# Kernel optimization log

Measured on AMD Instinct MI355X. Metric: run time of the kernel, lower is better.

The kernel has to match this reference:

```python
import jax, jax.numpy as jnp
import numpy as np


def setup_inputs() -> dict:
    key = jax.random.key(0)
    k1, k2, k3, k4 = jax.random.split(key, 4)
    B, N, M, C = 2, 16384, 4096, 64
    xyz = jax.random.uniform(k1, (B * N, 3), dtype=jnp.float32) * 10.0
    new_xyz = jax.random.uniform(k2, (B * M, 3), dtype=jnp.float32) * 10.0
    new_xyz_r = jax.random.uniform(k3, (B * M, 1), dtype=jnp.float32) * 0.6 + 0.4
    features = jax.random.normal(k4, (B * N, C), dtype=jnp.float32)
    xyz_batch_cnt = jnp.full((B,), N, dtype=jnp.int32)
    new_xyz_batch_cnt = jnp.full((B,), M, dtype=jnp.int32)
    return {
        "xyz": xyz,
        "xyz_batch_cnt": xyz_batch_cnt,
        "new_xyz": new_xyz,
        "new_xyz_r": new_xyz_r,
        "new_xyz_batch_cnt": new_xyz_batch_cnt,
        "features": features,
        "nsample": 32,
    }


def _ball_query(xyz_b, q_b, r_b, nsample):
    # xyz_b: (B, N, 3), q_b: (B, M, 3), r_b: (B, M)
    # Returns local neighbor indices (B, M, nsample) and empty-ball mask (B, M).
    B, N, _ = xyz_b.shape
    d2 = jnp.sum((q_b[:, :, None, :] - xyz_b[:, None, :, :]) ** 2, axis=-1)  # (B,M,N)
    within = d2 < (r_b[..., None] ** 2)  # (B,M,N)
    # key = point index if within ball else N -> top_k(-key) picks the FIRST
    # nsample in-ball indices in ascending order (matches CUDA ball query).
    pt_idx = jnp.arange(N, dtype=jnp.int32)
    key = jnp.where(within, pt_idx[None, None, :], jnp.int32(N))
    neg_vals, sel = jax.lax.top_k(-key, nsample)  # sel: (B,M,nsample) positions
    count = jnp.sum(within, axis=-1)  # (B,M)
    slot = jnp.arange(nsample, dtype=jnp.int32)
    valid = slot[None, None, :] < count[..., None]
    first = sel[..., 0:1]
    idx = jnp.where(valid, sel, first)  # pad with first found index
    empty = count == 0
    idx = jnp.where(empty[..., None], 0, idx).astype(jnp.int32)
    return idx, empty


def reference(xyz, xyz_batch_cnt, new_xyz, new_xyz_r, new_xyz_batch_cnt, features, nsample):
    B = xyz_batch_cnt.shape[0]
    N = xyz.shape[0] // B  # assumes equal batch counts
    M = new_xyz.shape[0] // B
    C = features.shape[1]
    xyz_b = xyz.reshape(B, N, 3)
    q_b = new_xyz.reshape(B, M, 3)
    r_b = new_xyz_r.reshape(B, M)
    feat_b = features.reshape(B, N, C)

    idx, empty = _ball_query(xyz_b, q_b, r_b, nsample)  # (B,M,ns), (B,M)

    gather = jax.vmap(lambda pts, i: pts[i])  # per-batch gather
    gx = gather(xyz_b, idx)  # (B,M,ns,3)
    grouped_xyz = jnp.transpose(gx, (0, 1, 3, 2)) - q_b[:, :, :, None]  # (B,M,3,ns)
    grouped_xyz = jnp.where(empty[:, :, None, None], 0.0, grouped_xyz)

    gf = gather(feat_b, idx)  # (B,M,ns,C)
    grouped_features = jnp.transpose(gf, (0, 1, 3, 2))  # (B,M,C,ns)
    grouped_features = jnp.where(empty[:, :, None, None], 0.0, grouped_features)

    new_features = jnp.concatenate([grouped_xyz, grouped_features], axis=2)  # use_xyz
    new_features = new_features.reshape(B * M, 3 + C, nsample)
    idx_flat = idx.reshape(B * M, nsample)
    return new_features, idx_flat
```

## Files before the change

kernel.cpp:

```cpp
#include <hip/hip_runtime.h>
#include <hip/hip_bf16.h>

#define NS   32
#define WPB  4
#define GD   10
#define GD3  (GD*GD*GD)
#define CAP  256
#define IMAX 0x7fffffff

__device__ __forceinline__ int clampi(int v, int lo, int hi) {
    return v < lo ? lo : (v > hi ? hi : v);
}

__device__ __forceinline__ int cell_of(float x, float y, float z) {
    const int cx = clampi((int)floorf(x), 0, GD - 1);
    const int cy = clampi((int)floorf(y), 0, GD - 1);
    const int cz = clampi((int)floorf(z), 0, GD - 1);
    return (cz * GD + cy) * GD + cx;
}

__device__ __forceinline__ float dist2_xla(float qx, float qy, float qz,
                                           float x, float y, float z) {
    const float dx = __fsub_rn(qx, x);
    const float dy = __fsub_rn(qy, y);
    const float dz = __fsub_rn(qz, z);
    return __fadd_rn(__fadd_rn(__fmul_rn(dx, dx), __fmul_rn(dy, dy)),
                     __fmul_rn(dz, dz));
}

__device__ __forceinline__ void find_batch(const int* cnts, int B, int p,
                                           int* b_out, int* off_out) {
    int b = 0, off = 0, acc = 0;
    for (int i = 0; i < B; ++i) {
        int c = cnts[i];
        if (p >= acc) { b = i; off = acc; }
        acc += c;
    }
    *b_out = b; *off_out = off;
}


__global__ void count_kernel(const float* __restrict__ xyz,
                             const int* __restrict__ xyz_cnt,
                             int* __restrict__ cnt, int B, int Ntot) {
    const int p = blockIdx.x * blockDim.x + threadIdx.x;
    if (p >= Ntot) return;
    int b, boff; find_batch(xyz_cnt, B, p, &b, &boff);
    const float x = xyz[(size_t)p * 3 + 0];
    const float y = xyz[(size_t)p * 3 + 1];
    const float z = xyz[(size_t)p * 3 + 2];
    atomicAdd(&cnt[b * GD3 + cell_of(x, y, z)], 1);
}

__global__ __launch_bounds__(1024) void prefix_kernel(int* __restrict__ cursor,
                                                      int* __restrict__ cell_start,
                                                      int ncells) {
    __shared__ int s[2048];
    const int t = threadIdx.x;
    for (int i = t; i < 2048; i += 1024) s[i] = (i < ncells) ? cursor[i] : 0;
    __syncthreads();
    for (int off = 1; off < 2048; off <<= 1) {
        const int v0 = s[t];
        const int a0 = (t >= off) ? s[t - off] : 0;
        const int v1 = s[t + 1024];
        const int a1 = s[t + 1024 - off];
        __syncthreads();
        s[t] = v0 + a0;
        s[t + 1024] = v1 + a1;
        __syncthreads();
    }
    for (int i = t; i < ncells; i += 1024) {
        const int excl = (i == 0) ? 0 : s[i - 1];
        cell_start[i] = excl;
        cursor[i]     = excl;
    }
    if (t == 0) cell_start[ncells] = s[ncells - 1];
}

__global__ void scatter_kernel(const float* __restrict__ xyz,
                               const int* __restrict__ xyz_cnt,
                               int* __restrict__ cursor,
                               float4* __restrict__ sorted,
                               int B, int Ntot) {
    const int p = blockIdx.x * blockDim.x + threadIdx.x;
    if (p >= Ntot) return;
    int b, boff; find_batch(xyz_cnt, B, p, &b, &boff);
    const float x = xyz[(size_t)p * 3 + 0];
    const float y = xyz[(size_t)p * 3 + 1];
    const float z = xyz[(size_t)p * 3 + 2];
    const int cell = b * GD3 + cell_of(x, y, z);
    const int slot = atomicAdd(&cursor[cell], 1);
    sorted[slot] = make_float4(x, y, z, __int_as_float(p - boff));
}


__global__ __launch_bounds__(256) void qgp_kernel(
    const float* __restrict__ xyz,
    const int*   __restrict__ xyz_cnt,
    const float* __restrict__ nxyz,
    const float* __restrict__ nr,
    const int*   __restrict__ nxyz_cnt,
    const float* __restrict__ feat,
    const int*   __restrict__ cell_start,
    const float4* __restrict__ sorted,
    float* __restrict__ out_feat,
    float* __restrict__ out_idx,
    int B, int Mtot, int C)
{
    __shared__ int c_list[WPB][CAP];
    __shared__ int idx_buf[WPB][NS];

    const int wv   = threadIdx.x >> 6;
    const int lane = threadIdx.x & 63;
    const int q    = blockIdx.x * WPB + wv;
    if (q >= Mtot) return;

    int b, qoff; find_batch(nxyz_cnt, B, q, &b, &qoff);
    int xoff; { int acc = 0; xoff = 0;
        for (int i = 0; i < B; ++i) { int c = xyz_cnt[i]; if (i == b) xoff = acc; acc += c; } }
    const float* xb = xyz + (size_t)xoff * 3;

    const float qx = nxyz[(size_t)q * 3 + 0];
    const float qy = nxyz[(size_t)q * 3 + 1];
    const float qz = nxyz[(size_t)q * 3 + 2];
    const float r  = nr[q];
    const float r2 = __fmul_rn(r, r);

    const float re = r + 1e-4f;
    const int cx0 = clampi((int)floorf(qx - re), 0, GD - 1);
    const int cx1 = clampi((int)floorf(qx + re), 0, GD - 1);
    const int cy0 = clampi((int)floorf(qy - re), 0, GD - 1);
    const int cy1 = clampi((int)floorf(qy + re), 0, GD - 1);
    const int cz0 = clampi((int)floorf(qz - re), 0, GD - 1);
    const int cz1 = clampi((int)floorf(qz + re), 0, GD - 1);
    const int cbase = b * GD3;

    const unsigned long long lane_mask = (1ull << lane) - 1ull;

    int n = 0;
    for (int cz = cz0; cz <= cz1; ++cz) {
        for (int cy = cy0; cy <= cy1; ++cy) {
            const int rb = cbase + (cz * GD + cy) * GD;
            const int s0 = cell_start[rb + cx0];
            const int s1 = cell_start[rb + cx1 + 1];
            for (int k0 = s0; k0 < s1; k0 += 64) {
                const int k = k0 + lane;
                bool ok = false; int ib = 0;
                if (k < s1) {
                    const float4 P = sorted[k];
                    ok = dist2_xla(qx, qy, qz, P.x, P.y, P.z) < r2;
                    ib = __float_as_int(P.w);
                }
                const unsigned long long m = __ballot(ok);
                if (ok) {
                    const int pos = n + __popcll(m & lane_mask);
                    if (pos < CAP) c_list[wv][pos] = ib;
                }
                n += __popcll(m);
            }
        }
    }
    if (n > CAP) n = CAP;
    __builtin_amdgcn_wave_barrier();

    int c0 = (lane       < n) ? c_list[wv][lane      ] : IMAX;
    int c1 = (lane +  64 < n) ? c_list[wv][lane +  64] : IMAX;
    int c2 = (lane + 128 < n) ? c_list[wv][lane + 128] : IMAX;
    int c3 = (lane + 192 < n) ? c_list[wv][lane + 192] : IMAX;
    const int filled = n < NS ? n : NS;
    for (int i = 0; i < filled; ++i) {
        const int mv = min(min(c0, c1), min(c2, c3));
        int w = mv;
#pragma unroll
        for (int d = 1; d < 64; d <<= 1) w = min(w, __shfl_xor(w, d));
        if (lane == i) idx_buf[wv][i] = w;
        const unsigned long long mm = __ballot(mv == w);
        const int first = __ffsll((unsigned long long)mm) - 1;
        if (lane == first) {
            if      (c0 == w) c0 = IMAX;
            else if (c1 == w) c1 = IMAX;
            else if (c2 == w) c2 = IMAX;
            else              c3 = IMAX;
        }
    }
    __builtin_amdgcn_wave_barrier();

    const bool empty = (n == 0);
    const int cnt32  = filled;
    const int s = lane & 31;
    const int h = lane >> 5;

    int sidx = 0;
    if (!empty) sidx = idx_buf[wv][(s < cnt32) ? s : 0];

    const size_t ob = (size_t)q * (size_t)(3 + C) * NS;

    if (h == 0) {
        out_idx[(size_t)q * NS + s] = (float)sidx;
        float px = 0.f, py = 0.f, pz = 0.f;
        if (!empty) {
            px = __fsub_rn(xb[(size_t)sidx * 3 + 0], qx);
            py = __fsub_rn(xb[(size_t)sidx * 3 + 1], qy);
            pz = __fsub_rn(xb[(size_t)sidx * 3 + 2], qz);
        }
        out_feat[ob + 0 * NS + s] = px;
        out_feat[ob + 1 * NS + s] = py;
        out_feat[ob + 2 * NS + s] = pz;
    }

    const float* frow = feat + (size_t)(xoff + sidx) * C;
    if (C == 64) {
        const float4* frow4 = reinterpret_cast<const float4*>(frow);
#pragma unroll
        for (int j = 0; j < 8; ++j) {
            float4 f;
            if (empty) { f.x = f.y = f.z = f.w = 0.f; }
            else       { f = frow4[h * 8 + j]; }
            const int cb = 3 + h * 32 + j * 4;
            out_feat[ob + (size_t)(cb + 0) * NS + s] = f.x;
            out_feat[ob + (size_t)(cb + 1) * NS + s] = f.y;
            out_feat[ob + (size_t)(cb + 2) * NS + s] = f.z;
            out_feat[ob + (size_t)(cb + 3) * NS + s] = f.w;
        }
    } else {
        for (int c = h; c < C; c += 2) {
            out_feat[ob + (size_t)(3 + c) * NS + s] = empty ? 0.f : frow[c];
        }
    }
}


__global__ __launch_bounds__(256) void qgp_scan_kernel(
    const float* __restrict__ xyz, const int* __restrict__ xyz_cnt,
    const float* __restrict__ nxyz, const float* __restrict__ nr,
    const int* __restrict__ nxyz_cnt, const float* __restrict__ feat,
    float* __restrict__ out_feat, float* __restrict__ out_idx,
    int B, int Mtot, int C)
{
    __shared__ int idx_buf[WPB][NS];
    const int wv = threadIdx.x >> 6, lane = threadIdx.x & 63;
    const int q = blockIdx.x * WPB + wv;
    if (q >= Mtot) return;
    int b, qoff; find_batch(nxyz_cnt, B, q, &b, &qoff);
    int xoff = 0, npts = 0; { int acc = 0;
        for (int i = 0; i < B; ++i) { int c = xyz_cnt[i]; if (i == b) { xoff = acc; npts = c; } acc += c; } }
    const float* xb = xyz + (size_t)xoff * 3;
    const float qx = nxyz[(size_t)q*3], qy = nxyz[(size_t)q*3+1], qz = nxyz[(size_t)q*3+2];
    const float r = nr[q], r2 = __fmul_rn(r, r);
    const unsigned long long lane_mask = (1ull << lane) - 1ull;
    int cnt = 0;
    for (int base = 0; base < npts && cnt < NS; base += 64) {
        const int k = base + lane;
        bool ok = false;
        if (k < npts)
            ok = dist2_xla(qx,qy,qz, xb[(size_t)k*3], xb[(size_t)k*3+1], xb[(size_t)k*3+2]) < r2;
        const unsigned long long m = __ballot(ok);
        if (ok) { const int pos = cnt + __popcll(m & lane_mask); if (pos < NS) idx_buf[wv][pos] = k; }
        cnt += __popcll(m);
    }
    __builtin_amdgcn_wave_barrier();
    const bool empty = (cnt == 0);
    const int cnt32 = cnt < NS ? cnt : NS;
    const int s = lane & 31, h = lane >> 5;
    int sidx = 0;
    if (!empty) sidx = idx_buf[wv][(s < cnt32) ? s : 0];
    const size_t ob = (size_t)q * (size_t)(3 + C) * NS;
    if (h == 0) {
        out_idx[(size_t)q * NS + s] = (float)sidx;
        float px=0.f, py=0.f, pz=0.f;
        if (!empty) {
            px = __fsub_rn(xb[(size_t)sidx*3+0], qx);
            py = __fsub_rn(xb[(size_t)sidx*3+1], qy);
            pz = __fsub_rn(xb[(size_t)sidx*3+2], qz);
        }
        out_feat[ob + 0*NS + s] = px; out_feat[ob + 1*NS + s] = py; out_feat[ob + 2*NS + s] = pz;
    }
    const float* frow = feat + (size_t)(xoff + sidx) * C;
    for (int c = h; c < C; c += 2)
        out_feat[ob + (size_t)(3 + c) * NS + s] = empty ? 0.f : frow[c];
}

extern "C" void kernel_launch(void* const* d_in, const int* in_sizes, int n_in,
                              void* d_out, int out_size, void* d_ws, size_t ws_size,
                              hipStream_t stream) {
    const float* xyz      = (const float*)d_in[0];
    const int*   xyz_cnt  = (const int*)d_in[1];
    const float* nxyz     = (const float*)d_in[2];
    const float* nr       = (const float*)d_in[3];
    const int*   nxyz_cnt = (const int*)d_in[4];
    const float* feat     = (const float*)d_in[5];

    const int B    = in_sizes[1];
    const int Ntot = in_sizes[0] / 3;
    const int Mtot = in_sizes[2] / 3;
    const int C    = in_sizes[5] / Ntot;

    float* out_feat = (float*)d_out;
    float* out_idx  = out_feat + (size_t)Mtot * (size_t)(3 + C) * NS;

    const int ncells = B * GD3;
    const size_t off_start  = 0;
    const size_t off_cursor = ((size_t)(ncells + 1) * 4 + 255) & ~(size_t)255;
    const size_t off_sorted = (off_cursor + (size_t)ncells * 4 + 255) & ~(size_t)255;
    const size_t need       = off_sorted + (size_t)Ntot * sizeof(float4);

    const bool grid_ok = (ws_size >= need) && (ncells + 1 <= 2048);

    if (grid_ok) {
        char* ws = (char*)d_ws;
        int*    cell_start = (int*)(ws + off_start);
        int*    cursor     = (int*)(ws + off_cursor);
        float4* sorted     = (float4*)(ws + off_sorted);

        hipMemsetAsync(cursor, 0, (size_t)ncells * 4, stream);
        count_kernel<<<(Ntot + 255) / 256, 256, 0, stream>>>(xyz, xyz_cnt, cursor, B, Ntot);
        prefix_kernel<<<1, 1024, 0, stream>>>(cursor, cell_start, ncells);
        scatter_kernel<<<(Ntot + 255) / 256, 256, 0, stream>>>(xyz, xyz_cnt, cursor, sorted, B, Ntot);
        qgp_kernel<<<(Mtot + WPB - 1) / WPB, 256, 0, stream>>>(
            xyz, xyz_cnt, nxyz, nr, nxyz_cnt, feat, cell_start, sorted,
            out_feat, out_idx, B, Mtot, C);
    } else {
        qgp_scan_kernel<<<(Mtot + WPB - 1) / WPB, 256, 0, stream>>>(
            xyz, xyz_cnt, nxyz, nr, nxyz_cnt, feat, out_feat, out_idx, B, Mtot, C);
    }
}
```

Before: 135.3 us.

## Replace candidate list and iterative min-selection with per-wave LDS bitmap

In-ball point indices are now marked with LDS atomicOr into a per-wave bitmap of 1024 words. A lane-wise popcount and a wave prefix scan then pull out the first NS indices in ascending order. This replaces the compacted candidate list and the up-to-32-round shuffle min-reduction, and drops the CAP=256 truncation. The cost is zeroing and reading 4KB of LDS per wave, LDS atomics, 16KB of LDS per block, and a new limit of Ntot<=32768 for taking the grid path.

```diff
diff --git a/kernel.cpp b/kernel.cpp
--- a/kernel.cpp
+++ b/kernel.cpp
@@ -5,8 +5,7 @@
 #define WPB  4
 #define GD   10
 #define GD3  (GD*GD*GD)
-#define CAP  256
-#define IMAX 0x7fffffff
+#define BMW  1024
 
 __device__ __forceinline__ int clampi(int v, int lo, int hi) {
     return v < lo ? lo : (v > hi ? hi : v);
@@ -93,7 +92,6 @@
     sorted[slot] = make_float4(x, y, z, __int_as_float(p - boff));
 }
 
-
 __global__ __launch_bounds__(256) void qgp_kernel(
     const float* __restrict__ xyz,
     const int*   __restrict__ xyz_cnt,
@@ -107,13 +105,16 @@
     float* __restrict__ out_idx,
     int B, int Mtot, int C)
 {
-    __shared__ int c_list[WPB][CAP];
+    __shared__ unsigned bm[WPB][BMW];
     __shared__ int idx_buf[WPB][NS];
 
     const int wv   = threadIdx.x >> 6;
     const int lane = threadIdx.x & 63;
     const int q    = blockIdx.x * WPB + wv;
     if (q >= Mtot) return;
+
+#pragma unroll
+    for (int t = 0; t < BMW / 64; ++t) bm[wv][lane + 64 * t] = 0u;
 
     int b, qoff; find_batch(nxyz_cnt, B, q, &b, &qoff);
     int xoff; { int acc = 0; xoff = 0;
@@ -135,9 +136,8 @@
     const int cz1 = clampi((int)floorf(qz + re), 0, GD - 1);
     const int cbase = b * GD3;
 
-    const unsigned long long lane_mask = (1ull << lane) - 1ull;
-
-    int n = 0;
+    __builtin_amdgcn_wave_barrier();
+
     for (int cz = cz0; cz <= cz1; ++cz) {
         for (int cy = cy0; cy <= cy1; ++cy) {
             const int rb = cbase + (cz * GD + cy) * GD;
@@ -145,48 +145,50 @@
             const int s1 = cell_start[rb + cx1 + 1];
             for (int k0 = s0; k0 < s1; k0 += 64) {
                 const int k = k0 + lane;
-                bool ok = false; int ib = 0;
                 if (k < s1) {
                     const float4 P = sorted[k];
-                    ok = dist2_xla(qx, qy, qz, P.x, P.y, P.z) < r2;
-                    ib = __float_as_int(P.w);
+                    if (dist2_xla(qx, qy, qz, P.x, P.y, P.z) < r2) {
+                        const int ib = __float_as_int(P.w);
+                        const int wi = ib >> 5;
+                        atomicOr(&bm[wv][((wi & 15) << 6) + (wi >> 4)],
+                                 1u << (ib & 31));
+                    }
                 }
-                const unsigned long long m = __ballot(ok);
-                if (ok) {
-                    const int pos = n + __popcll(m & lane_mask);
-                    if (pos < CAP) c_list[wv][pos] = ib;
-                }
-                n += __popcll(m);
             }
         }
     }
-    if (n > CAP) n = CAP;
     __builtin_amdgcn_wave_barrier();
 
-    int c0 = (lane       < n) ? c_list[wv][lane      ] : IMAX;
-    int c1 = (lane +  64 < n) ? c_list[wv][lane +  64] : IMAX;
-    int c2 = (lane + 128 < n) ? c_list[wv][lane + 128] : IMAX;
-    int c3 = (lane + 192 < n) ? c_list[wv][lane + 192] : IMAX;
-    const int filled = n < NS ? n : NS;
-    for (int i = 0; i < filled; ++i) {
-        const int mv = min(min(c0, c1), min(c2, c3));
-        int w = mv;
+    unsigned words[16];
+    int mytot = 0;
 #pragma unroll
-        for (int d = 1; d < 64; d <<= 1) w = min(w, __shfl_xor(w, d));
-        if (lane == i) idx_buf[wv][i] = w;
-        const unsigned long long mm = __ballot(mv == w);
-        const int first = __ffsll((unsigned long long)mm) - 1;
-        if (lane == first) {
-            if      (c0 == w) c0 = IMAX;
-            else if (c1 == w) c1 = IMAX;
-            else if (c2 == w) c2 = IMAX;
-            else              c3 = IMAX;
+    for (int j = 0; j < 16; ++j) {
+        words[j] = bm[wv][(j << 6) + lane];
+        mytot += __popc(words[j]);
+    }
+    int incl = mytot;
+#pragma unroll
+    for (int d = 1; d < 64; d <<= 1) {
+        const int v = __shfl_up(incl, d);
+        if (lane >= d) incl += v;
+    }
+    const int total = __shfl(incl, 63);
+    int pos = incl - mytot;
+    if (pos < NS) {
+        for (int j = 0; j < 16 && pos < NS; ++j) {
+            unsigned w = words[j];
+            while (w && pos < NS) {
+                const int bit = __ffs(w) - 1;
+                idx_buf[wv][pos] = (lane << 9) + (j << 5) + bit;
+                ++pos;
+                w &= w - 1;
+            }
         }
     }
     __builtin_amdgcn_wave_barrier();
 
-    const bool empty = (n == 0);
-    const int cnt32  = filled;
+    const bool empty = (total == 0);
+    const int cnt32  = total < NS ? total : NS;
     const int s = lane & 31;
     const int h = lane >> 5;
 
@@ -304,7 +306,8 @@
     const size_t off_sorted = (off_cursor + (size_t)ncells * 4 + 255) & ~(size_t)255;
     const size_t need       = off_sorted + (size_t)Ntot * sizeof(float4);
 
-    const bool grid_ok = (ws_size >= need) && (ncells + 1 <= 2048);
+    const bool grid_ok = (ws_size >= need) && (ncells + 1 <= 2048) &&
+                         (Ntot <= BMW * 32);
 
     if (grid_ok) {
         char* ws = (char*)d_ws;
```

Result: no change. 133.0 us (-1.7%).
